# Optimization experiments

Measured on AMD Instinct MI355X. Metric: run time of the kernel, lower is better.

Reference implementation:

```python
import jax, jax.numpy as jnp
import numpy as np

N_NODES = 10000
N_EDGES = 160000
HIDDEN = 64
NUM_RBF = 32
Q_DIM = 8
CUTOFF_UPPER = 5.0


def silu(x):
    return x * jax.nn.sigmoid(x)


def tensor_norm(X):
    # X: [n, 3, 3, H] -> [n, H] (Frobenius norm squared over the 3x3 dims)
    return (X * X).sum(axis=(1, 2))


def decompose_tensor(X):
    # X: [n, 3, 3, H] -> I: [n, H] (trace/3), A: antisym [n,3,3,H], S: sym traceless [n,3,3,H]
    eye = jnp.eye(3, dtype=X.dtype)[None, :, :, None]
    I = jnp.einsum('naah->nh', X) / 3.0
    Xt = X.transpose(0, 2, 1, 3)
    A = 0.5 * (X - Xt)
    S = 0.5 * (X + Xt) - I[:, None, None, :] * eye
    return I, A, S


def compose_tensor(I, A, S):
    eye = jnp.eye(3, dtype=A.dtype)[None, :, :, None]
    return I[:, None, None, :] * eye + A + S


def tmm(P, Q):
    # 3x3 matmul per (atom, channel): [n,3,3,H] x [n,3,3,H] -> [n,3,3,H]
    return jnp.einsum('nach,ncbh->nabh', P, Q)


def setup_inputs() -> dict:
    key = jax.random.key(0)
    ks = jax.random.split(key, 16)
    H = HIDDEN
    inp = {
        'X': jax.random.normal(ks[0], (N_NODES, 3, 3, H), jnp.float32),
        'charges': jax.random.normal(ks[1], (N_NODES, Q_DIM), jnp.float32),
        'edge_weight': jax.random.uniform(ks[2], (N_EDGES,), jnp.float32) * CUTOFF_UPPER,
        'edge_attr': jax.random.normal(ks[3], (N_EDGES, NUM_RBF), jnp.float32),
        'edge_index': jax.random.randint(ks[4], (2, N_EDGES), 0, N_NODES, jnp.int32),
    }
    d_in = NUM_RBF + 2 * Q_DIM
    inp['Ws1'] = jax.random.normal(ks[5], (d_in, H), jnp.float32) / np.sqrt(d_in).astype(np.float32)
    inp['bs1'] = jnp.zeros((H,), jnp.float32)
    inp['Ws2'] = jax.random.normal(ks[6], (H, 2 * H), jnp.float32) / np.sqrt(H).astype(np.float32)
    inp['bs2'] = jnp.zeros((2 * H,), jnp.float32)
    inp['Ws3'] = jax.random.normal(ks[7], (2 * H, 3 * H), jnp.float32) / np.sqrt(2 * H).astype(np.float32)
    inp['bs3'] = jnp.zeros((3 * H,), jnp.float32)
    for i in range(6):
        inp['Wt%d' % i] = jax.random.normal(ks[8 + i], (H, H), jnp.float32) / np.sqrt(H).astype(np.float32)
    return inp


def reference(X, charges, edge_weight, edge_attr, Ws1, bs1, Ws2, bs2, Ws3, bs3,
              Wt0, Wt1, Wt2, Wt3, Wt4, Wt5, edge_index):
    H = HIDDEN
    n = X.shape[0]
    row, col = edge_index[0], edge_index[1]
    # cosine cutoff (cutoff_lower = 0)
    C = 0.5 * (jnp.cos(edge_weight * (jnp.pi / CUTOFF_UPPER)) + 1.0)
    C = C * (edge_weight < CUTOFF_UPPER).astype(X.dtype)
    # edge scalar MLP on [rbf, q_i, q_j]
    h = jnp.concatenate([edge_attr, charges[row], charges[col]], axis=-1)
    h = silu(h @ Ws1 + bs1)
    h = silu(h @ Ws2 + bs2)
    h = silu(h @ Ws3 + bs3)
    w = (h * C[:, None]).reshape(h.shape[0], 3, H)  # [E, 3, H]
    # normalize node tensors
    X = X / (tensor_norm(X) + 1.0)[:, None, None, :]
    I, A, S = decompose_tensor(X)
    I = I @ Wt0
    A = A @ Wt1
    S = S @ Wt2
    Y = compose_tensor(I, A, S)
    # message passing: gather I/A/S at source (edge_index[1]), weight per component, scatter-add at dest (edge_index[0])
    eye = jnp.eye(3, dtype=X.dtype)[None, :, :, None]
    msg_e = ((w[:, 0] * I[col])[:, None, None, :] * eye
             + w[:, 1][:, None, None, :] * A[col]
             + w[:, 2][:, None, None, :] * S[col])  # [E, 3, 3, H]
    msg = jax.ops.segment_sum(msg_e, row, num_segments=n)  # [n, 3, 3, H]
    # O(3): C = msg @ Y + Y @ msg (3x3 matmul per channel)
    Cm = tmm(msg, Y) + tmm(Y, msg)
    I2, A2, S2 = decompose_tensor(Cm)
    normp1 = tensor_norm(Cm) + 1.0
    I2 = I2 / normp1
    A2 = A2 / normp1[:, None, None, :]
    S2 = S2 / normp1[:, None, None, :]
    I2 = I2 @ Wt3
    A2 = A2 @ Wt4
    S2 = S2 @ Wt5
    dX = compose_tensor(I2, A2, S2)
    return X + dX + tmm(dX, dX)
```

## Files before the change

kernel.cpp:

```cpp
#include <hip/hip_runtime.h>
#include <math.h>

#define HD 64

typedef _Float16 half8 __attribute__((ext_vector_type(8)));
typedef _Float16 half4v __attribute__((ext_vector_type(4)));
typedef float floatx4 __attribute__((ext_vector_type(4)));

__device__ __forceinline__ float silu_f(float x) {
    return x * __builtin_amdgcn_rcpf(1.0f + __expf(-x));
}

__global__ __launch_bounds__(256) void node_pre(
    const float* __restrict__ X,
    const float* __restrict__ Wt0, const float* __restrict__ Wt1, const float* __restrict__ Wt2,
    float* __restrict__ Tn, _Float16* __restrict__ TnH, int N)
{
    int sub = threadIdx.x >> 6;
    int h = threadIdx.x & 63;
    int n = blockIdx.x * 4 + sub;
    int nn = (n < N) ? n : (N - 1);

    const float* Xb = X + (size_t)nn * 9 * HD + h;
    float x[9];
    float nrm = 0.f;
#pragma unroll
    for (int i = 0; i < 9; ++i) { x[i] = Xb[i * HD]; nrm += x[i] * x[i]; }
    float inv = 1.0f / (nrm + 1.0f);
#pragma unroll
    for (int i = 0; i < 9; ++i) x[i] *= inv;

    float I0 = (x[0] + x[4] + x[8]) * (1.0f / 3.0f);
    __shared__ float comp[4][10][HD];
    comp[sub][0][h] = I0;
    comp[sub][1][h] = 0.5f * (x[1] - x[3]);
    comp[sub][2][h] = 0.5f * (x[2] - x[6]);
    comp[sub][3][h] = 0.5f * (x[5] - x[7]);
    comp[sub][4][h] = x[0] - I0;
    comp[sub][5][h] = 0.5f * (x[1] + x[3]);
    comp[sub][6][h] = 0.5f * (x[2] + x[6]);
    comp[sub][7][h] = x[4] - I0;
    comp[sub][8][h] = 0.5f * (x[5] + x[7]);
    comp[sub][9][h] = x[8] - I0;
    __syncthreads();
    float acc[10];
#pragma unroll
    for (int i = 0; i < 10; ++i) acc[i] = 0.f;
    for (int k = 0; k < HD; ++k) {
        float w0 = Wt0[k * HD + h];
        float w1 = Wt1[k * HD + h];
        float w2 = Wt2[k * HD + h];
        acc[0] += comp[sub][0][k] * w0;
        acc[1] += comp[sub][1][k] * w1;
        acc[2] += comp[sub][2][k] * w1;
        acc[3] += comp[sub][3][k] * w1;
#pragma unroll
        for (int j = 0; j < 6; ++j) acc[4 + j] += comp[sub][4 + j][k] * w2;
    }
    if (n < N) {
        float* tp = Tn + (size_t)n * 640 + h;
        _Float16* th = TnH + (size_t)n * 640 + h;
#pragma unroll
        for (int i = 0; i < 10; ++i) {
            tp[i * 64] = acc[i];
            th[i * 64] = (_Float16)acc[i];
        }
    }
}

__global__ __launch_bounds__(256) void count_kernel(
    const int* __restrict__ edge_index, int* __restrict__ cnt, int E)
{
    int e = blockIdx.x * 256 + threadIdx.x;
    if (e < E) atomicAdd(&cnt[edge_index[e]], 1);
}

__global__ __launch_bounds__(1024) void scan_kernel(
    const int* __restrict__ cnt, int* __restrict__ offs, int* __restrict__ curs, int N)
{
    __shared__ int partials[16];
    __shared__ int base_s;
    int tid = threadIdx.x, wid = tid >> 6, lane = tid & 63;
    if (tid == 0) base_s = 0;
    __syncthreads();
    for (int start = 0; start < N; start += 1024) {
        int i = start + tid;
        int v = (i < N) ? cnt[i] : 0;
        int s = v;
#pragma unroll
        for (int d = 1; d < 64; d <<= 1) {
            int t = __shfl_up(s, d, 64);
            if (lane >= d) s += t;
        }
        if (lane == 63) partials[wid] = s;
        __syncthreads();
        if (tid == 0) {
            int run = base_s;
#pragma unroll
            for (int w = 0; w < 16; ++w) { int t = partials[w]; partials[w] = run; run += t; }
            base_s = run;
        }
        __syncthreads();
        int excl = partials[wid] + s - v;
        if (i < N) { offs[i] = excl; curs[i] = excl; }
        __syncthreads();
    }
    if (tid == 0) offs[N] = base_s;
}

__global__ __launch_bounds__(256) void place_kernel(
    const int* __restrict__ edge_index, int* __restrict__ curs,
    int* __restrict__ rank, int* __restrict__ colP, int E)
{
    int e = blockIdx.x * 256 + threadIdx.x;
    if (e < E) {
        int p = atomicAdd(&curs[edge_index[e]], 1);
        rank[e] = p;
        colP[p] = edge_index[E + e];
    }
}

__global__ __launch_bounds__(256) void wconv(
    const float* __restrict__ Ws1, const float* __restrict__ Ws2, const float* __restrict__ Ws3,
    _Float16* __restrict__ W1f, _Float16* __restrict__ W2f, _Float16* __restrict__ W3f)
{
    int id = blockIdx.x * 256 + threadIdx.x;
    if (id < 4096) {
        int i = id & 7, l = (id >> 3) & 63, t = id >> 9;
        int s = t >> 2, nt = t & 3;
        int k = s * 32 + (l >> 4) * 8 + i;
        int n = nt * 16 + (l & 15);
        W1f[id] = (k < 48) ? (_Float16)Ws1[k * 64 + n] : (_Float16)0.f;
    } else if (id < 4096 + 8192) {
        int j = id - 4096;
        int i = j & 7, l = (j >> 3) & 63, t = j >> 9;
        int s = t >> 3, nt = t & 7;
        int k = s * 32 + (l >> 4) * 8 + i;
        int n = nt * 16 + (l & 15);
        W2f[j] = (_Float16)Ws2[k * 128 + n];
    } else if (id < 4096 + 8192 + 24576) {
        int j = id - 4096 - 8192;
        int i = j & 7, l = (j >> 3) & 63, t = j >> 9;
        int s = t / 12, nt = t % 12;
        int k = s * 32 + (l >> 4) * 8 + i;
        int n = nt * 16 + (l & 15);
        W3f[j] = (_Float16)Ws3[k * 192 + n];
    }
}

__global__ __launch_bounds__(256, 6) void mlp_mfma(
    const float* __restrict__ edge_attr, const float* __restrict__ charges,
    const float* __restrict__ edge_weight, const int* __restrict__ edge_index,
    const int* __restrict__ rank,
    const _Float16* __restrict__ W1f, const float* __restrict__ bs1,
    const _Float16* __restrict__ W2f, const float* __restrict__ bs2,
    const _Float16* __restrict__ W3f, const float* __restrict__ bs3,
    _Float16* __restrict__ bufH, int E)
{
    __shared__ __align__(16) _Float16 act[4][16][208];
    __shared__ float cvsS[4][16];
    __shared__ int rankSS[4][16];

    int tid = threadIdx.x;
    int wv = tid >> 6, l = tid & 63;
    int base = blockIdx.x * 64 + wv * 16;
    int row16 = l & 15, quad = l >> 4;

#pragma unroll
    for (int i = 0; i < 4; ++i) {
        int slot = l + i * 64;
        int e_l = slot >> 4, f = slot & 15;
        int e = base + e_l;
        int ee = (e < E) ? e : (E - 1);
        float4 v = make_float4(0.f, 0.f, 0.f, 0.f);
        if (f < 8) {
            v = *(const float4*)(edge_attr + (size_t)ee * 32 + f * 4);
        } else if (f < 10) {
            int r = edge_index[ee];
            v = *(const float4*)(charges + (size_t)r * 8 + (f - 8) * 4);
        } else if (f < 12) {
            int c = edge_index[E + ee];
            v = *(const float4*)(charges + (size_t)c * 8 + (f - 10) * 4);
        }
        half4v hv = { (_Float16)v.x, (_Float16)v.y, (_Float16)v.z, (_Float16)v.w };
        *(half4v*)&act[wv][e_l][f * 4] = hv;
    }
    if (l < 16) {
        int e = base + l;
        int ee = (e < E) ? e : (E - 1);
        rankSS[wv][l] = rank[ee];
        float wgt = edge_weight[ee];
        float cv = 0.5f * (__cosf(wgt * 0.6283185307179586f) + 1.0f);
        cvsS[wv][l] = (wgt < 5.0f) ? cv : 0.0f;
    }

    half8 A[4];
    A[0] = *(const half8*)&act[wv][row16][quad * 8];
    A[1] = *(const half8*)&act[wv][row16][32 + quad * 8];
    floatx4 acc1[4];
#pragma unroll
    for (int nt = 0; nt < 4; ++nt) {
        floatx4 c = {0.f, 0.f, 0.f, 0.f};
        c = __builtin_amdgcn_mfma_f32_16x16x32_f16(
                A[0], *(const half8*)(W1f + ((size_t)(0 * 4 + nt) * 64 + l) * 8), c, 0, 0, 0);
        c = __builtin_amdgcn_mfma_f32_16x16x32_f16(
                A[1], *(const half8*)(W1f + ((size_t)(1 * 4 + nt) * 64 + l) * 8), c, 0, 0, 0);
        acc1[nt] = c;
    }
#pragma unroll
    for (int nt = 0; nt < 4; ++nt) {
        float b = bs1[nt * 16 + row16];
#pragma unroll
        for (int r = 0; r < 4; ++r)
            act[wv][quad * 4 + r][64 + nt * 16 + row16] = (_Float16)silu_f(acc1[nt][r] + b);
    }

    A[0] = *(const half8*)&act[wv][row16][64 + quad * 8];
    A[1] = *(const half8*)&act[wv][row16][96 + quad * 8];
    floatx4 acc2[8];
#pragma unroll
    for (int nt = 0; nt < 8; ++nt) {
        floatx4 c = {0.f, 0.f, 0.f, 0.f};
        c = __builtin_amdgcn_mfma_f32_16x16x32_f16(
                A[0], *(const half8*)(W2f + ((size_t)(0 * 8 + nt) * 64 + l) * 8), c, 0, 0, 0);
        c = __builtin_amdgcn_mfma_f32_16x16x32_f16(
                A[1], *(const half8*)(W2f + ((size_t)(1 * 8 + nt) * 64 + l) * 8), c, 0, 0, 0);
        acc2[nt] = c;
    }
#pragma unroll
    for (int nt = 0; nt < 8; ++nt) {
        float b = bs2[nt * 16 + row16];
#pragma unroll
        for (int r = 0; r < 4; ++r)
            act[wv][quad * 4 + r][nt * 16 + row16] = (_Float16)silu_f(acc2[nt][r] + b);
    }

    A[0] = *(const half8*)&act[wv][row16][quad * 8];
    A[1] = *(const half8*)&act[wv][row16][32 + quad * 8];
    A[2] = *(const half8*)&act[wv][row16][64 + quad * 8];
    A[3] = *(const half8*)&act[wv][row16][96 + quad * 8];

    float cvrow[4];
#pragma unroll
    for (int r = 0; r < 4; ++r) cvrow[r] = cvsS[wv][quad * 4 + r];

    floatx4 acc3[12];
#pragma unroll
    for (int nt = 0; nt < 12; ++nt) {
        floatx4 c = {0.f, 0.f, 0.f, 0.f};
#pragma unroll
        for (int s = 0; s < 4; ++s)
            c = __builtin_amdgcn_mfma_f32_16x16x32_f16(
                    A[s], *(const half8*)(W3f + ((size_t)(s * 12 + nt) * 64 + l) * 8), c, 0, 0, 0);
        acc3[nt] = c;
    }
#pragma unroll
    for (int nt = 0; nt < 12; ++nt) {
        float b = bs3[nt * 16 + row16];
#pragma unroll
        for (int r = 0; r < 4; ++r)
            act[wv][quad * 4 + r][nt * 16 + row16] =
                (_Float16)(silu_f(acc3[nt][r] + b) * cvrow[r]);
    }
    {
        int fr = l >> 2;
        int ef = base + fr;
        if (ef < E) {
            _Float16* dst = bufH + (size_t)rankSS[wv][fr] * 192;
#pragma unroll
            for (int i = 0; i < 6; ++i) {
                int j = (l & 3) + i * 4;
                *(half8*)(dst + j * 8) = *(const half8*)&act[wv][fr][j * 8];
            }
        }
    }
}

__global__ __launch_bounds__(256) void msg_kernel(
    const _Float16* __restrict__ bufH, const int* __restrict__ colP,
    const int* __restrict__ offs, const _Float16* __restrict__ TnH,
    float* __restrict__ Mn, int N)
{
    int n = blockIdx.x * 2 + (threadIdx.x >> 7);
    if (n >= N) return;
    int half = (threadIdx.x >> 6) & 1;
    int lane = threadIdx.x & 63;
    int beg = offs[n], end = offs[n + 1];

    if (half == 0) {
        float a0 = 0.f, a1 = 0.f, a2 = 0.f, a3 = 0.f;
#pragma unroll 4
        for (int idx = beg; idx < end; ++idx) {
            int c = colP[idx];
            const _Float16* wp = bufH + (size_t)idx * 192;
            float w0 = (float)wp[lane];
            float w1 = (float)wp[64 + lane];
            const _Float16* tp = TnH + (size_t)c * 640;
            a0 += w0 * (float)tp[lane];
            a1 += w1 * (float)tp[64 + lane];
            a2 += w1 * (float)tp[128 + lane];
            a3 += w1 * (float)tp[192 + lane];
        }
        float* mp = Mn + (size_t)n * 640;
        mp[lane] = a0;
        mp[64 + lane] = a1; mp[128 + lane] = a2; mp[192 + lane] = a3;
    } else {
        float a4 = 0.f, a5 = 0.f, a6 = 0.f, a7 = 0.f, a8 = 0.f, a9 = 0.f;
#pragma unroll 4
        for (int idx = beg; idx < end; ++idx) {
            int c = colP[idx];
            const _Float16* wp = bufH + (size_t)idx * 192;
            float w2 = (float)wp[128 + lane];
            const _Float16* tp = TnH + (size_t)c * 640;
            a4 += w2 * (float)tp[256 + lane];
            a5 += w2 * (float)tp[320 + lane];
            a6 += w2 * (float)tp[384 + lane];
            a7 += w2 * (float)tp[448 + lane];
            a8 += w2 * (float)tp[512 + lane];
            a9 += w2 * (float)tp[576 + lane];
        }
        float* mp = Mn + (size_t)n * 640;
        mp[256 + lane] = a4; mp[320 + lane] = a5; mp[384 + lane] = a6;
        mp[448 + lane] = a7; mp[512 + lane] = a8; mp[576 + lane] = a9;
    }
}

__global__ __launch_bounds__(256) void node_post(
    const float* __restrict__ X,
    const float* __restrict__ Tn, const float* __restrict__ Mn,
    const float* __restrict__ Wt3, const float* __restrict__ Wt4, const float* __restrict__ Wt5,
    float* __restrict__ out, int N)
{
    int sub = threadIdx.x >> 6;
    int h = threadIdx.x & 63;
    int n = blockIdx.x * 4 + sub;
    int nn = (n < N) ? n : (N - 1);

    const float* Xb = X + (size_t)nn * 9 * HD + h;
    float x[9];
    float nr = 0.f;
#pragma unroll
    for (int i = 0; i < 9; ++i) { x[i] = Xb[i * HD]; nr += x[i] * x[i]; }
    float xinv = 1.0f / (nr + 1.0f);
#pragma unroll
    for (int i = 0; i < 9; ++i) x[i] *= xinv;

    const float* tp = Tn + (size_t)nn * 640 + h;
    const float* mp = Mn + (size_t)nn * 640 + h;
    float yI = tp[0], mI = mp[0];
    float yA[3], yS[6], mA[3], mS[6];
#pragma unroll
    for (int j = 0; j < 3; ++j) { yA[j] = tp[(1 + j) * 64]; mA[j] = mp[(1 + j) * 64]; }
#pragma unroll
    for (int j = 0; j < 6; ++j) { yS[j] = tp[(4 + j) * 64]; mS[j] = mp[(4 + j) * 64]; }

    float M[3][3] = {
        { mI + mS[0],     mA[0] + mS[1],   mA[1] + mS[2] },
        { -mA[0] + mS[1], mI + mS[3],      mA[2] + mS[4] },
        { -mA[1] + mS[2], -mA[2] + mS[4],  mI + mS[5] } };
    float Y[3][3] = {
        { yI + yS[0],     yA[0] + yS[1],   yA[1] + yS[2] },
        { -yA[0] + yS[1], yI + yS[3],      yA[2] + yS[4] },
        { -yA[1] + yS[2], -yA[2] + yS[4],  yI + yS[5] } };

    float Cm[3][3];
    float nrm = 0.f;
#pragma unroll
    for (int a = 0; a < 3; ++a) {
#pragma unroll
        for (int b = 0; b < 3; ++b) {
            float s = 0.f;
#pragma unroll
            for (int c = 0; c < 3; ++c) s += M[a][c] * Y[c][b] + Y[a][c] * M[c][b];
            Cm[a][b] = s;
            nrm += s * s;
        }
    }
    float inv = 1.0f / (nrm + 1.0f);
    float tr3 = (Cm[0][0] + Cm[1][1] + Cm[2][2]) * (1.0f / 3.0f);

    __shared__ float comp[4][10][HD];
    comp[sub][0][h] = tr3 * inv;
    comp[sub][1][h] = 0.5f * (Cm[0][1] - Cm[1][0]) * inv;
    comp[sub][2][h] = 0.5f * (Cm[0][2] - Cm[2][0]) * inv;
    comp[sub][3][h] = 0.5f * (Cm[1][2] - Cm[2][1]) * inv;
    comp[sub][4][h] = (Cm[0][0] - tr3) * inv;
    comp[sub][5][h] = 0.5f * (Cm[0][1] + Cm[1][0]) * inv;
    comp[sub][6][h] = 0.5f * (Cm[0][2] + Cm[2][0]) * inv;
    comp[sub][7][h] = (Cm[1][1] - tr3) * inv;
    comp[sub][8][h] = 0.5f * (Cm[1][2] + Cm[2][1]) * inv;
    comp[sub][9][h] = (Cm[2][2] - tr3) * inv;
    __syncthreads();

    float acc[10];
#pragma unroll
    for (int i = 0; i < 10; ++i) acc[i] = 0.f;
    for (int k = 0; k < HD; ++k) {
        float w3 = Wt3[k * HD + h];
        float w4 = Wt4[k * HD + h];
        float w5 = Wt5[k * HD + h];
        acc[0] += comp[sub][0][k] * w3;
        acc[1] += comp[sub][1][k] * w4;
        acc[2] += comp[sub][2][k] * w4;
        acc[3] += comp[sub][3][k] * w4;
#pragma unroll
        for (int j = 0; j < 6; ++j) acc[4 + j] += comp[sub][4 + j][k] * w5;
    }
    float D[3][3] = {
        { acc[0] + acc[4],  acc[1] + acc[5],  acc[2] + acc[6] },
        { -acc[1] + acc[5], acc[0] + acc[7],  acc[3] + acc[8] },
        { -acc[2] + acc[6], -acc[3] + acc[8], acc[0] + acc[9] } };

    if (n < N) {
        float* ob = out + (size_t)n * 9 * HD + h;
#pragma unroll
        for (int a = 0; a < 3; ++a) {
#pragma unroll
            for (int b = 0; b < 3; ++b) {
                float s = 0.f;
#pragma unroll
                for (int c = 0; c < 3; ++c) s += D[a][c] * D[c][b];
                ob[(a * 3 + b) * HD] = x[a * 3 + b] + D[a][b] + s;
            }
        }
    }
}

extern "C" void kernel_launch(void* const* d_in, const int* in_sizes, int n_in,
                              void* d_out, int out_size, void* d_ws, size_t ws_size,
                              hipStream_t stream)
{
    const float* X           = (const float*)d_in[0];
    const float* charges     = (const float*)d_in[1];
    const float* edge_weight = (const float*)d_in[2];
    const float* edge_attr   = (const float*)d_in[3];
    const int*   edge_index  = (const int*)d_in[4];
    const float* Ws1 = (const float*)d_in[5];
    const float* bs1 = (const float*)d_in[6];
    const float* Ws2 = (const float*)d_in[7];
    const float* bs2 = (const float*)d_in[8];
    const float* Ws3 = (const float*)d_in[9];
    const float* bs3 = (const float*)d_in[10];
    const float* Wt0 = (const float*)d_in[11];
    const float* Wt1 = (const float*)d_in[12];
    const float* Wt2 = (const float*)d_in[13];
    const float* Wt3 = (const float*)d_in[14];
    const float* Wt4 = (const float*)d_in[15];
    const float* Wt5 = (const float*)d_in[16];

    int N = in_sizes[0] / (9 * HD);
    int E = in_sizes[2];

    float* ws = (float*)d_ws;
    float* Tn  = ws;
    float* Mn  = Tn + (size_t)N * 640;
    _Float16* TnH  = (_Float16*)(Mn + (size_t)N * 640);
    _Float16* bufH = TnH + (size_t)N * 640;
    int* cnt   = (int*)(bufH + (size_t)E * 192);
    int* offs  = cnt + N;
    int* curs  = offs + N + 1;
    int* rank  = curs + N;
    int* colP  = rank + E;
    size_t fofs = ((size_t)((char*)(colP + E) - (char*)d_ws) + 15) & ~(size_t)15;
    _Float16* W1f = (_Float16*)((char*)d_ws + fofs);
    _Float16* W2f = W1f + 4096;
    _Float16* W3f = W2f + 8192;

    hipMemsetAsync(cnt, 0, (size_t)N * sizeof(int), stream);

    int nbE256 = (E + 255) / 256;
    count_kernel<<<nbE256, 256, 0, stream>>>(edge_index, cnt, E);
    scan_kernel<<<1, 1024, 0, stream>>>(cnt, offs, curs, N);
    place_kernel<<<nbE256, 256, 0, stream>>>(edge_index, curs, rank, colP, E);

    wconv<<<144, 256, 0, stream>>>(Ws1, Ws2, Ws3, W1f, W2f, W3f);

    node_pre<<<(N + 3) / 4, 256, 0, stream>>>(X, Wt0, Wt1, Wt2, Tn, TnH, N);

    int nbE64 = (E + 63) / 64;
    mlp_mfma<<<nbE64, 256, 0, stream>>>(edge_attr, charges, edge_weight, edge_index,
                                        rank, W1f, bs1, W2f, bs2, W3f, bs3, bufH, E);

    msg_kernel<<<(N + 1) / 2, 256, 0, stream>>>(bufH, colP, offs, TnH, Mn, N);

    node_post<<<(N + 3) / 4, 256, 0, stream>>>(X, Tn, Mn, Wt3, Wt4, Wt5, (float*)d_out, N);
}
```

Before: 184.3 us.

## Fuse message aggregation with node post-processing and retune MLP occupancy

Merges msg_kernel and node_post into a single msg_post kernel that keeps the per-node aggregated message in shared memory instead of writing and rereading a global Mn buffer. This removes one launch and the Mn round trip through memory. In exchange, both waves of each node slot redundantly compute the post-processing and only half of them store results, so half the threads do wasted work in the post phase. Separately, the MLP kernel's launch-bounds occupancy hint drops from 6 to 4 and the shared activation row padding shrinks from 208 to 200.

```diff
diff --git a/kernel.cpp b/kernel.cpp
--- a/kernel.cpp
+++ b/kernel.cpp
@@ -148,7 +148,7 @@
     }
 }
 
-__global__ __launch_bounds__(256, 6) void mlp_mfma(
+__global__ __launch_bounds__(256, 4) void mlp_mfma(
     const float* __restrict__ edge_attr, const float* __restrict__ charges,
     const float* __restrict__ edge_weight, const int* __restrict__ edge_index,
     const int* __restrict__ rank,
@@ -157,7 +157,7 @@
     const _Float16* __restrict__ W3f, const float* __restrict__ bs3,
     _Float16* __restrict__ bufH, int E)
 {
-    __shared__ __align__(16) _Float16 act[4][16][208];
+    __shared__ __align__(16) _Float16 act[4][16][200];
     __shared__ float cvsS[4][16];
     __shared__ int rankSS[4][16];
 
@@ -276,16 +276,22 @@
     }
 }
 
-__global__ __launch_bounds__(256) void msg_kernel(
+__global__ __launch_bounds__(256) void msg_post(
     const _Float16* __restrict__ bufH, const int* __restrict__ colP,
     const int* __restrict__ offs, const _Float16* __restrict__ TnH,
-    float* __restrict__ Mn, int N)
-{
-    int n = blockIdx.x * 2 + (threadIdx.x >> 7);
-    if (n >= N) return;
+    const float* __restrict__ Tn, const float* __restrict__ X,
+    const float* __restrict__ Wt3, const float* __restrict__ Wt4, const float* __restrict__ Wt5,
+    float* __restrict__ out, int N)
+{
+    __shared__ float MnS[2][10][64];
+    __shared__ float comp[2][10][64];
+
+    int slot = threadIdx.x >> 7;
     int half = (threadIdx.x >> 6) & 1;
     int lane = threadIdx.x & 63;
-    int beg = offs[n], end = offs[n + 1];
+    int n = blockIdx.x * 2 + slot;
+    int nn = (n < N) ? n : (N - 1);
+    int beg = offs[nn], end = offs[nn + 1];
 
     if (half == 0) {
         float a0 = 0.f, a1 = 0.f, a2 = 0.f, a3 = 0.f;
@@ -301,9 +307,8 @@
             a2 += w1 * (float)tp[128 + lane];
             a3 += w1 * (float)tp[192 + lane];
         }
-        float* mp = Mn + (size_t)n * 640;
-        mp[lane] = a0;
-        mp[64 + lane] = a1; mp[128 + lane] = a2; mp[192 + lane] = a3;
+        MnS[slot][0][lane] = a0; MnS[slot][1][lane] = a1;
+        MnS[slot][2][lane] = a2; MnS[slot][3][lane] = a3;
     } else {
         float a4 = 0.f, a5 = 0.f, a6 = 0.f, a7 = 0.f, a8 = 0.f, a9 = 0.f;
 #pragma unroll 4
@@ -319,23 +324,13 @@
             a8 += w2 * (float)tp[512 + lane];
             a9 += w2 * (float)tp[576 + lane];
         }
-        float* mp = Mn + (size_t)n * 640;
-        mp[256 + lane] = a4; mp[320 + lane] = a5; mp[384 + lane] = a6;
-        mp[448 + lane] = a7; mp[512 + lane] = a8; mp[576 + lane] = a9;
-    }
-}
-
-__global__ __launch_bounds__(256) void node_post(
-    const float* __restrict__ X,
-    const float* __restrict__ Tn, const float* __restrict__ Mn,
-    const float* __restrict__ Wt3, const float* __restrict__ Wt4, const float* __restrict__ Wt5,
-    float* __restrict__ out, int N)
-{
-    int sub = threadIdx.x >> 6;
-    int h = threadIdx.x & 63;
-    int n = blockIdx.x * 4 + sub;
-    int nn = (n < N) ? n : (N - 1);
-
+        MnS[slot][4][lane] = a4; MnS[slot][5][lane] = a5;
+        MnS[slot][6][lane] = a6; MnS[slot][7][lane] = a7;
+        MnS[slot][8][lane] = a8; MnS[slot][9][lane] = a9;
+    }
+    __syncthreads();
+
+    int h = lane;
     const float* Xb = X + (size_t)nn * 9 * HD + h;
     float x[9];
     float nr = 0.f;
@@ -346,13 +341,12 @@
     for (int i = 0; i < 9; ++i) x[i] *= xinv;
 
     const float* tp = Tn + (size_t)nn * 640 + h;
-    const float* mp = Mn + (size_t)nn * 640 + h;
-    float yI = tp[0], mI = mp[0];
+    float yI = tp[0], mI = MnS[slot][0][h];
     float yA[3], yS[6], mA[3], mS[6];
 #pragma unroll
-    for (int j = 0; j < 3; ++j) { yA[j] = tp[(1 + j) * 64]; mA[j] = mp[(1 + j) * 64]; }
-#pragma unroll
-    for (int j = 0; j < 6; ++j) { yS[j] = tp[(4 + j) * 64]; mS[j] = mp[(4 + j) * 64]; }
+    for (int j = 0; j < 3; ++j) { yA[j] = tp[(1 + j) * 64]; mA[j] = MnS[slot][1 + j][h]; }
+#pragma unroll
+    for (int j = 0; j < 6; ++j) { yS[j] = tp[(4 + j) * 64]; mS[j] = MnS[slot][4 + j][h]; }
 
     float M[3][3] = {
         { mI + mS[0],     mA[0] + mS[1],   mA[1] + mS[2] },
@@ -379,17 +373,18 @@
     float inv = 1.0f / (nrm + 1.0f);
     float tr3 = (Cm[0][0] + Cm[1][1] + Cm[2][2]) * (1.0f / 3.0f);
 
-    __shared__ float comp[4][10][HD];
-    comp[sub][0][h] = tr3 * inv;
-    comp[sub][1][h] = 0.5f * (Cm[0][1] - Cm[1][0]) * inv;
-    comp[sub][2][h] = 0.5f * (Cm[0][2] - Cm[2][0]) * inv;
-    comp[sub][3][h] = 0.5f * (Cm[1][2] - Cm[2][1]) * inv;
-    comp[sub][4][h] = (Cm[0][0] - tr3) * inv;
-    comp[sub][5][h] = 0.5f * (Cm[0][1] + Cm[1][0]) * inv;
-    comp[sub][6][h] = 0.5f * (Cm[0][2] + Cm[2][0]) * inv;
-    comp[sub][7][h] = (Cm[1][1] - tr3) * inv;
-    comp[sub][8][h] = 0.5f * (Cm[1][2] + Cm[2][1]) * inv;
-    comp[sub][9][h] = (Cm[2][2] - tr3) * inv;
+    if (half == 0) {
+        comp[slot][0][h] = tr3 * inv;
+        comp[slot][1][h] = 0.5f * (Cm[0][1] - Cm[1][0]) * inv;
+        comp[slot][2][h] = 0.5f * (Cm[0][2] - Cm[2][0]) * inv;
+        comp[slot][3][h] = 0.5f * (Cm[1][2] - Cm[2][1]) * inv;
+        comp[slot][4][h] = (Cm[0][0] - tr3) * inv;
+        comp[slot][5][h] = 0.5f * (Cm[0][1] + Cm[1][0]) * inv;
+        comp[slot][6][h] = 0.5f * (Cm[0][2] + Cm[2][0]) * inv;
+        comp[slot][7][h] = (Cm[1][1] - tr3) * inv;
+        comp[slot][8][h] = 0.5f * (Cm[1][2] + Cm[2][1]) * inv;
+        comp[slot][9][h] = (Cm[2][2] - tr3) * inv;
+    }
     __syncthreads();
 
     float acc[10];
@@ -399,19 +394,19 @@
         float w3 = Wt3[k * HD + h];
         float w4 = Wt4[k * HD + h];
         float w5 = Wt5[k * HD + h];
-        acc[0] += comp[sub][0][k] * w3;
-        acc[1] += comp[sub][1][k] * w4;
-        acc[2] += comp[sub][2][k] * w4;
-        acc[3] += comp[sub][3][k] * w4;
-#pragma unroll
-        for (int j = 0; j < 6; ++j) acc[4 + j] += comp[sub][4 + j][k] * w5;
+        acc[0] += comp[slot][0][k] * w3;
+        acc[1] += comp[slot][1][k] * w4;
+        acc[2] += comp[slot][2][k] * w4;
+        acc[3] += comp[slot][3][k] * w4;
+#pragma unroll
+        for (int j = 0; j < 6; ++j) acc[4 + j] += comp[slot][4 + j][k] * w5;
     }
     float D[3][3] = {
         { acc[0] + acc[4],  acc[1] + acc[5],  acc[2] + acc[6] },
         { -acc[1] + acc[5], acc[0] + acc[7],  acc[3] + acc[8] },
         { -acc[2] + acc[6], -acc[3] + acc[8], acc[0] + acc[9] } };
 
-    if (n < N) {
+    if (half == 0 && n < N) {
         float* ob = out + (size_t)n * 9 * HD + h;
 #pragma unroll
         for (int a = 0; a < 3; ++a) {
@@ -453,8 +448,7 @@
 
     float* ws = (float*)d_ws;
     float* Tn  = ws;
-    float* Mn  = Tn + (size_t)N * 640;
-    _Float16* TnH  = (_Float16*)(Mn + (size_t)N * 640);
+    _Float16* TnH  = (_Float16*)(Tn + (size_t)N * 640);
     _Float16* bufH = TnH + (size_t)N * 640;
     int* cnt   = (int*)(bufH + (size_t)E * 192);
     int* offs  = cnt + N;
@@ -481,7 +475,6 @@
     mlp_mfma<<<nbE64, 256, 0, stream>>>(edge_attr, charges, edge_weight, edge_index,
                                         rank, W1f, bs1, W2f, bs2, W3f, bs3, bufH, E);
 
-    msg_kernel<<<(N + 1) / 2, 256, 0, stream>>>(bufH, colP, offs, TnH, Mn, N);
-
-    node_post<<<(N + 3) / 4, 256, 0, stream>>>(X, Tn, Mn, Wt3, Wt4, Wt5, (float*)d_out, N);
-}
+    msg_post<<<(N + 1) / 2, 256, 0, stream>>>(bufH, colP, offs, TnH, Tn, X,
+                                              Wt3, Wt4, Wt5, (float*)d_out, N);
+}
```

Result: slower. 190.8 us (+3.5%).
